# Kernel optimization log

Measured on AMD Instinct MI355X. Metric: run time of the kernel, lower is better.

The kernel has to match this reference:

```python
import jax, jax.numpy as jnp
import numpy as np

PRE_NMS_TOPK = 6000
POST_NMS_TOPK = 1000
NMS_THRESH = 0.7
MIN_SIZE = 16.0
NEG = -1e9  # stand-in for -inf that is safe under autodiff


def setup_inputs() -> dict:
    key = jax.random.key(0)
    k1, k2, k3, k4, k5, k6, k7, k8 = jax.random.split(key, 8)
    B, A = 8, 200000
    N = B * A
    # realistic anchors: centers within a ~1333x800 canvas, sizes 16..256
    cx = jax.random.uniform(k1, (N,), minval=0.0, maxval=1200.0)
    cy = jax.random.uniform(k2, (N,), minval=0.0, maxval=800.0)
    w = jax.random.uniform(k3, (N,), minval=16.0, maxval=256.0)
    h = jax.random.uniform(k4, (N,), minval=16.0, maxval=256.0)
    anchors = jnp.stack([cx - 0.5 * w, cy - 0.5 * h, cx + 0.5 * w, cy + 0.5 * h], axis=1)
    batch_indices = jnp.sort(jax.random.randint(k5, (N,), 0, B)).astype(jnp.int32)
    image_sizes = jax.random.randint(k6, (B, 2), 600, 1334).astype(jnp.int32)  # (H, W)
    objectness_logits = jax.random.normal(k7, (N, 1), dtype=jnp.float32)
    bbox_deltas = jax.random.normal(k8, (N, 4), dtype=jnp.float32) * 0.2
    return {
        'anchors': anchors,
        'batch_indices': batch_indices,
        'image_sizes': image_sizes,
        'objectness_logits': objectness_logits,
        'bbox_deltas': bbox_deltas,
    }


def _nms_one(bx, sc):
    """Greedy NMS on [K,4] boxes / [K] scores; returns POST_NMS_TOPK (idx, ok)."""
    K = bx.shape[0]
    areas = (bx[:, 2] - bx[:, 0]) * (bx[:, 3] - bx[:, 1])
    ar = jnp.arange(K)

    def step(sup, _):
        s = jnp.where(sup, NEG, sc)
        j = jnp.argmax(s)
        ok = s[j] > 0.5 * NEG
        b = bx[j]
        ix1 = jnp.maximum(b[0], bx[:, 0])
        iy1 = jnp.maximum(b[1], bx[:, 1])
        ix2 = jnp.minimum(b[2], bx[:, 2])
        iy2 = jnp.minimum(b[3], bx[:, 3])
        inter = jnp.maximum(ix2 - ix1, 0.0) * jnp.maximum(iy2 - iy1, 0.0)
        iou = inter / (areas + areas[j] - inter + 1e-9)
        sup = sup | (iou > NMS_THRESH) | (ar == j)
        return sup, (j, ok)

    sup0 = sc <= 0.5 * NEG  # padded / invalid entries start suppressed
    _, (idx, ok) = jax.lax.scan(step, sup0, None, length=POST_NMS_TOPK)
    return idx, ok


def reference(anchors, batch_indices, image_sizes, objectness_logits, bbox_deltas):
    B = image_sizes.shape[0]
    N = anchors.shape[0]
    sizes = image_sizes[batch_indices].astype(jnp.float32)  # [N,2] (H,W) per anchor

    # --- box decode ---
    a_w = anchors[:, 2] - anchors[:, 0]
    a_h = anchors[:, 3] - anchors[:, 1]
    a_x = anchors[:, 0] + 0.5 * a_w
    a_y = anchors[:, 1] + 0.5 * a_h
    t_x, t_y = bbox_deltas[:, 0], bbox_deltas[:, 1]
    t_w, t_h = bbox_deltas[:, 2], bbox_deltas[:, 3]
    p_x = a_x + t_x * a_w
    p_y = a_y + t_y * a_h
    p_w = a_w * jnp.exp(jnp.clip(t_w, -10.0, 10.0))
    p_h = a_h * jnp.exp(jnp.clip(t_h, -10.0, 10.0))
    x1 = p_x - 0.5 * p_w
    y1 = p_y - 0.5 * p_h
    x2 = p_x + 0.5 * p_w
    y2 = p_y + 0.5 * p_h

    # --- clip to image ---
    H, W = sizes[:, 0], sizes[:, 1]
    x1 = jnp.clip(x1, 0.0, W - 1.0)
    y1 = jnp.clip(y1, 0.0, H - 1.0)
    x2 = jnp.clip(x2, 0.0, W - 1.0)
    y2 = jnp.clip(y2, 0.0, H - 1.0)
    boxes = jnp.stack([x1, y1, x2, y2], axis=1)  # [N,4]

    # --- min-size filter (as score masking) ---
    valid = ((x2 - x1) >= MIN_SIZE) & ((y2 - y1) >= MIN_SIZE)
    fg = jax.nn.sigmoid(objectness_logits[:, 0])

    # --- per-image top-k over masked scores ---
    img_mask = batch_indices[None, :] == jnp.arange(B, dtype=batch_indices.dtype)[:, None]  # [B,N]
    scores = jnp.where(img_mask & valid[None, :], fg[None, :], NEG)  # [B,N]
    top_scores, top_idx = jax.lax.top_k(scores, PRE_NMS_TOPK)  # [B,PRE]
    top_boxes = boxes[top_idx]  # [B,PRE,4]

    # --- NMS per image ---
    keep_idx, keep_ok = jax.vmap(_nms_one)(top_boxes, top_scores)  # [B,POST]

    sel = jnp.take_along_axis(top_idx, keep_idx, axis=1)  # global anchor indices [B,POST]
    okf = keep_ok[..., None].astype(boxes.dtype)
    props = jnp.take_along_axis(top_boxes, keep_idx[..., None], axis=1) * okf  # [B,POST,4]
    obj = objectness_logits[sel] * okf  # [B,POST,1]
    deltas_out = bbox_deltas[sel] * okf  # [B,POST,4]
    bidx = jnp.where(keep_ok, jnp.arange(B, dtype=jnp.int32)[:, None], -1)  # [B,POST]

    return (props.reshape(-1, 4), bidx.reshape(-1), obj.reshape(-1, 1),
            deltas_out.reshape(-1, 4), keep_ok.reshape(-1))
```

## Files before the change

### kernel.cpp

```cpp
#include <hip/hip_runtime.h>
#include <stdint.h>

#define PRE_K   6000
#define POST_K  1000
#define CAP     8192
#define BINS    1024
#define ROWS    6016
#define CH      94
#define RC_CH   32
#define JSPLIT  4
#define NEGF    -1000000000.0f
#define IOU_EPS 16.0f


__device__ __forceinline__ uint32_t orderf(float f) {
  uint32_t u = __float_as_uint(f);
  return (u & 0x80000000u) ? ~u : (u | 0x80000000u);
}

__device__ __forceinline__ int score_bin(float sc) {
  int bin = (int)floorf((sc + 12.0f) * ((float)BINS / 24.0f));
  return bin < 0 ? 0 : (bin > BINS - 1 ? BINS - 1 : bin);
}

__device__ __forceinline__ int bin_slot(int bin) {
  return ((bin & 15) << 6) | (bin >> 4);
}

__device__ __forceinline__ void decode_box(
    const float* __restrict__ anchors, const float* __restrict__ deltas,
    const int* __restrict__ isz, int n, int b,
    double& x1, double& y1, double& x2, double& y2, bool& valid) {
  double ax1 = (double)anchors[4 * n + 0], ay1 = (double)anchors[4 * n + 1];
  double ax2 = (double)anchors[4 * n + 2], ay2 = (double)anchors[4 * n + 3];
  double aw = ax2 - ax1, ah = ay2 - ay1;
  double acx = ax1 + 0.5 * aw, acy = ay1 + 0.5 * ah;
  double tx = (double)deltas[4 * n + 0], ty = (double)deltas[4 * n + 1];
  double tw = (double)deltas[4 * n + 2], th = (double)deltas[4 * n + 3];
  tw = tw < -10.0 ? -10.0 : (tw > 10.0 ? 10.0 : tw);
  th = th < -10.0 ? -10.0 : (th > 10.0 ? 10.0 : th);
  double px = acx + tx * aw, py = acy + ty * ah;
  double pw = aw * exp(tw), ph = ah * exp(th);
  double H = (double)isz[2 * b + 0], W = (double)isz[2 * b + 1];
  double wm = W - 1.0, hm = H - 1.0;
  x1 = px - 0.5 * pw; y1 = py - 0.5 * ph;
  x2 = px + 0.5 * pw; y2 = py + 0.5 * ph;
  x1 = fmin(fmax(x1, 0.0), wm); x2 = fmin(fmax(x2, 0.0), wm);
  y1 = fmin(fmax(y1, 0.0), hm); y2 = fmin(fmax(y2, 0.0), hm);
  valid = (x2 - x1 >= 16.0) && (y2 - y1 >= 16.0);
}

__device__ __forceinline__ bool iou_exact(const double* __restrict__ tbox,
                                          const double* __restrict__ tarea,
                                          size_t ri, size_t ci) {
  const double* pr = &tbox[ri * 4];
  const double* pc = &tbox[ci * 4];
  double w = fmin(pr[2], pc[2]) - fmax(pr[0], pc[0]); w = w > 0.0 ? w : 0.0;
  double h = fmin(pr[3], pc[3]) - fmax(pr[1], pc[1]); h = h > 0.0 ? h : 0.0;
  double it = w * h;
  return it > 0.7 * (tarea[ri] + tarea[ci] - it + 1e-9);
}


__global__ void k_init(uint32_t* hist, uint32_t* cnt, uint32_t* prank, int B) {
  int i = blockIdx.x * blockDim.x + threadIdx.x;
  if (i < B * BINS) hist[i] = 0u;
  if (i < B) cnt[i] = 0u;
  if (i < B * CAP) prank[i] = 0u;
}

__global__ void __launch_bounds__(256) k_score(const float* __restrict__ anchors,
                                               const int* __restrict__ bix,
                                               const int* __restrict__ isz,
                                               const float* __restrict__ logits,
                                               const float* __restrict__ deltas,
                                               float* __restrict__ scores,
                                               uint32_t* __restrict__ hist, int N) {
  const int SPAN = 4096;
  int start = blockIdx.x * SPAN;
  int end = start + SPAN < N ? start + SPAN : N;
  __shared__ uint32_t lh[2][BINS];
  for (int i = threadIdx.x; i < 2 * BINS; i += 256) ((uint32_t*)lh)[i] = 0u;
  __shared__ int s_b0, s_b1;
  if (threadIdx.x == 0) { s_b0 = bix[start]; s_b1 = bix[end - 1]; }
  __syncthreads();
  int b0 = s_b0, b1 = s_b1;

  for (int n = start + (int)threadIdx.x; n < end; n += 256) {
    int b = bix[n];
    double x1, y1, x2, y2; bool valid;
    decode_box(anchors, deltas, isz, n, b, x1, y1, x2, y2, valid);
    float sc = valid ? logits[n] : NEGF;
    scores[n] = sc;
    if (valid) {
      int bin = score_bin(sc);
      if (b == b0)      atomicAdd(&lh[0][bin], 1u);
      else if (b == b1) atomicAdd(&lh[1][bin], 1u);
      else              atomicAdd(&hist[b * BINS + bin_slot(bin)], 1u);
    }
  }
  __syncthreads();
  for (int bin = threadIdx.x; bin < BINS; bin += 256) {
    uint32_t c0 = lh[0][bin];
    if (c0) atomicAdd(&hist[b0 * BINS + bin_slot(bin)], c0);
    if (b1 != b0) {
      uint32_t c1 = lh[1][bin];
      if (c1) atomicAdd(&hist[b1 * BINS + bin_slot(bin)], c1);
    }
  }
}

__global__ void k_scan(const uint32_t* __restrict__ hist, uint32_t* __restrict__ bstar) {
  __shared__ uint32_t s[BINS];
  __shared__ int bs;
  int b = blockIdx.x, t = threadIdx.x;
  s[t] = hist[b * BINS + bin_slot(t)];
  if (t == 0) bs = 0;
  __syncthreads();
  for (int off = 1; off < BINS; off <<= 1) {
    uint32_t v = (t + off < BINS) ? s[t + off] : 0u;
    __syncthreads();
    s[t] += v;
    __syncthreads();
  }
  if (s[t] >= PRE_K) atomicMax(&bs, t);
  __syncthreads();
  if (t == 0) bstar[b] = (uint32_t)bs;
}

__global__ void __launch_bounds__(1024) k_compact(const float* __restrict__ scores,
                                                  const int* __restrict__ bix,
                                                  const uint32_t* __restrict__ bstar,
                                                  uint32_t* __restrict__ cnt,
                                                  uint64_t* __restrict__ cand, int N) {
  const int SPAN = 8192;
  int start = blockIdx.x * SPAN;
  int end = start + SPAN < N ? start + SPAN : N;
  __shared__ uint32_t lcnt[8], lbase[8];
  if (threadIdx.x < 8) lcnt[threadIdx.x] = 0u;
  __syncthreads();

  bool     predv[8];
  uint64_t keyv[8];
  uint32_t lposv[8];
  int      bv[8];
  int nt = 0;
  for (int base = start; base < end; base += 1024, nt++) {
    int n = base + (int)threadIdx.x;
    bool pred = false; int b = 0; uint64_t key = 0ull; uint32_t lp = 0u;
    if (n < end) {
      float sc = scores[n];
      if (sc > 0.5f * NEGF) {
        b = bix[n];
        if ((uint32_t)score_bin(sc) >= bstar[b]) {
          pred = true;
          key = ((uint64_t)orderf(sc) << 32) | (uint64_t)(uint32_t)(~(uint32_t)n);
          lp = atomicAdd(&lcnt[b], 1u);
        }
      }
    }
    predv[nt] = pred; keyv[nt] = key; lposv[nt] = lp; bv[nt] = b;
  }
  __syncthreads();
  if (threadIdx.x < 8) {
    uint32_t c = lcnt[threadIdx.x];
    lbase[threadIdx.x] = c ? atomicAdd(&cnt[threadIdx.x], c) : 0u;
  }
  __syncthreads();
  for (int k = 0; k < nt; k++) {
    if (predv[k]) {
      uint32_t pos = lbase[bv[k]] + lposv[k];
      if (pos < CAP) cand[(size_t)bv[k] * CAP + pos] = keyv[k];
    }
  }
}

__global__ void __launch_bounds__(256) k_rank(const uint64_t* __restrict__ cand,
                                              const uint32_t* __restrict__ cnt,
                                              uint32_t* __restrict__ prank) {
  int blk = blockIdx.x;
  int js = blk % JSPLIT;
  int ic = (blk / JSPLIT) % 32;
  int b  = blk / (JSPLIT * 32);
  int t = threadIdx.x;
  int C = (int)min(cnt[b], (uint32_t)CAP);
  if (ic * 256 >= C) return;
  const uint64_t* g = cand + (size_t)b * CAP;
  int i = ic * 256 + t;
  uint64_t ki = (i < C) ? g[i] : 0ull;

  int q = (C + JSPLIT - 1) / JSPLIT;
  int j0 = js * q;
  int j1 = j0 + q < C ? j0 + q : C;
  if (j0 >= j1) return;

  __shared__ uint64_t tile[1024];
  int rank = 0;
  for (int base = j0; base < j1; base += 1024) {
#pragma unroll
    for (int u = 0; u < 4; u++) {
      int j = base + u * 256 + t;
      tile[u * 256 + t] = (j < j1) ? g[j] : 0ull;
    }
    __syncthreads();
    int lim = j1 - base < 1024 ? j1 - base : 1024;
    const ulonglong2* t2 = (const ulonglong2*)tile;
    int pairs = lim >> 1;
    int jj = 0;
    for (; jj + 4 <= pairs; jj += 4) {
      ulonglong2 v0 = t2[jj + 0], v1 = t2[jj + 1];
      ulonglong2 v2 = t2[jj + 2], v3 = t2[jj + 3];
      rank += (v0.x > ki) ? 1 : 0; rank += (v0.y > ki) ? 1 : 0;
      rank += (v1.x > ki) ? 1 : 0; rank += (v1.y > ki) ? 1 : 0;
      rank += (v2.x > ki) ? 1 : 0; rank += (v2.y > ki) ? 1 : 0;
      rank += (v3.x > ki) ? 1 : 0; rank += (v3.y > ki) ? 1 : 0;
    }
    for (; jj < pairs; jj++) {
      ulonglong2 v = t2[jj];
      rank += (v.x > ki) ? 1 : 0; rank += (v.y > ki) ? 1 : 0;
    }
    if (lim & 1) rank += (tile[lim - 1] > ki) ? 1 : 0;
    __syncthreads();
  }
  if (i < C && rank) atomicAdd(&prank[b * CAP + i], (uint32_t)rank);
}

__global__ void __launch_bounds__(256) k_place_gather(
    const uint64_t* __restrict__ cand, const uint32_t* __restrict__ cnt,
    const uint32_t* __restrict__ prank,
    const float* __restrict__ anchors, const float* __restrict__ deltas,
    const int* __restrict__ isz,
    double* __restrict__ tbox, double* __restrict__ tarea,
    float4* __restrict__ tboxf, float* __restrict__ tareaf,
    int* __restrict__ top_n, int* __restrict__ Cnum, int B) {
  int idx = blockIdx.x * blockDim.x + threadIdx.x;
  if (idx >= B * CAP) return;
  int b = idx / CAP, i = idx % CAP;
  int C = (int)min(cnt[b], (uint32_t)CAP);
  if (i == 0) Cnum[b] = C < PRE_K ? C : PRE_K;
  if (i >= C) return;
  uint32_t rank = prank[idx];
  if (rank >= PRE_K) return;
  int n = (int)(~(uint32_t)(cand[idx] & 0xFFFFFFFFull));
  double x1, y1, x2, y2; bool valid;
  decode_box(anchors, deltas, isz, n, b, x1, y1, x2, y2, valid);
  size_t row = (size_t)b * ROWS + rank;
  tbox[row * 4 + 0] = x1;
  tbox[row * 4 + 1] = y1;
  tbox[row * 4 + 2] = x2;
  tbox[row * 4 + 3] = y2;
  double ar = (x2 - x1) * (y2 - y1);
  tarea[row] = ar;
  tboxf[row] = make_float4((float)x1, (float)y1, (float)x2, (float)y2);
  tareaf[row] = (float)ar;
  top_n[b * PRE_K + rank] = n;
}

__global__ void __launch_bounds__(64) k_iou_mat(const float4* __restrict__ tboxf,
                                                const float* __restrict__ tareaf,
                                                const double* __restrict__ tbox,
                                                const double* __restrict__ tarea,
                                                const int* __restrict__ Cnum,
                                                uint32_t* __restrict__ maskT) {
  int blk = blockIdx.x;
  int k  = blk % (RC_CH + 1);
  int cc = (blk / (RC_CH + 1)) % CH;
  int b  = blk / ((RC_CH + 1) * CH);
  int rc = (k == RC_CH) ? cc : k;
  if (k < RC_CH && cc <= rc) return;
  int C = Cnum[b];
  if (rc * 64 >= C || cc * 64 >= C) return;
  int lane = threadIdx.x;
  size_t bb = (size_t)b * ROWS;

  float4 cb4 = tboxf[bb + (size_t)cc * 64 + lane];
  float  sca = 0.7f * tareaf[bb + (size_t)cc * 64 + lane];
  __shared__ float4 rbx[64];
  __shared__ float  rsa[64];
  rbx[lane] = tboxf[bb + (size_t)rc * 64 + lane];
  rsa[lane] = 0.7f * tareaf[bb + (size_t)rc * 64 + lane];
  __syncthreads();

  bool isdiag = (rc == cc);
  uint32_t res0 = 0u, res1 = 0u;

  for (int i = 0; i < 64; i++) {
    float4 r4 = rbx[i];
    float sra = rsa[i];
    float iw = fminf(r4.z, cb4.z) - fmaxf(r4.x, cb4.x);
    float ih = fminf(r4.w, cb4.w) - fmaxf(r4.y, cb4.y);
    iw = fmaxf(iw, 0.0f); ih = fmaxf(ih, 0.0f);
    float inter = iw * ih;
    float diff = fmaf(1.7f, inter, -(sra + sca));
    bool gt = isdiag ? (lane > i) : true;
    unsigned long long sup   = __ballot(gt && (diff >  IOU_EPS));
    unsigned long long loose = __ballot(gt && (diff > -IOU_EPS));
    unsigned long long border = loose & ~sup;
    if (border) {
      bool mine = (border >> lane) & 1ull;
      bool ex = false;
      if (mine)
        ex = iou_exact(tbox, tarea, bb + (size_t)rc * 64 + i,
                       bb + (size_t)cc * 64 + lane);
      sup |= __ballot(ex);
    }
    if (lane == i) { res0 = (uint32_t)sup; res1 = (uint32_t)(sup >> 32); }
  }
  uint2* seg = (uint2*)(maskT + (((size_t)b * CH + cc) * ROWS + (size_t)rc * 64) * 2);
  seg[lane] = make_uint2(res0, res1);
}

__global__ void __launch_bounds__(256) k_nms_reduce(const uint32_t* __restrict__ maskT,
                                                    const float4* __restrict__ tboxf,
                                                    const float* __restrict__ tareaf,
                                                    const double* __restrict__ tbox,
                                                    const double* __restrict__ tarea,
                                                    const int* __restrict__ Cnum,
                                                    int* __restrict__ keep,
                                                    int* __restrict__ kept_count) {
  int b = blockIdx.x, t = threadIdx.x;
  int wave = t >> 6, lane = t & 63;
  int C = Cnum[b];
  const uint32_t* M = maskT + (size_t)b * CH * ROWS * 2;
  size_t bb = (size_t)b * ROWS;

  __shared__ uint32_t s_f[2][2];
  __shared__ uint32_t kept_lo[POST_K];
  __shared__ uint32_t kept_hi[POST_K];
  __shared__ uint64_t s_kept;
  if (t < 4) ((uint32_t*)s_f)[t] = 0u;

  uint32_t d0 = 0u, d1 = 0u;
  if (wave == 0) {
    const uint32_t* rp = M + (size_t)lane * 2;
    d0 = rp[0]; d1 = rp[1];
  }
  __syncthreads();

  int nkept = 0, nlo = 0, nhi = 0;
  for (int c = 0; c < CH; c++) {
    int base = c * 64;
    if (base >= C) break;
    int cbuf = c & 1;
    if (t == 0) { s_f[cbuf ^ 1][0] = 0u; s_f[cbuf ^ 1][1] = 0u; }

    uint32_t f0 = 0u, f1 = 0u;
    for (int k2 = t; k2 < nlo; k2 += 256) {
      const uint32_t* rp = M + ((size_t)c * ROWS + kept_lo[k2]) * 2;
      f0 |= rp[0]; f1 |= rp[1];
    }
    if (nhi > 0) {
      float4 cb4 = tboxf[bb + base + lane];
      float  sca = 0.7f * tareaf[bb + base + lane];
      for (int k2 = wave; k2 < nhi; k2 += 4) {
        int r = (int)kept_hi[k2];
        float4 r4 = tboxf[bb + r];
        float sra = 0.7f * tareaf[bb + r];
        float iw = fminf(r4.z, cb4.z) - fmaxf(r4.x, cb4.x);
        float ih = fminf(r4.w, cb4.w) - fmaxf(r4.y, cb4.y);
        iw = fmaxf(iw, 0.0f); ih = fmaxf(ih, 0.0f);
        float inter = iw * ih;
        float diff = fmaf(1.7f, inter, -(sra + sca));
        unsigned long long sup   = __ballot(diff >  IOU_EPS);
        unsigned long long loose = __ballot(diff > -IOU_EPS);
        unsigned long long border = loose & ~sup;
        if (border) {
          bool mine = (border >> lane) & 1ull;
          bool ex = false;
          if (mine) ex = iou_exact(tbox, tarea, bb + r, bb + base + lane);
          sup |= __ballot(ex);
        }
        f0 |= (uint32_t)sup; f1 |= (uint32_t)(sup >> 32);
      }
    }
#pragma unroll
    for (int off = 32; off > 0; off >>= 1) {
      f0 |= (uint32_t)__shfl_xor((int)f0, off, 64);
      f1 |= (uint32_t)__shfl_xor((int)f1, off, 64);
    }
    if (lane == 0 && (f0 | f1)) {
      atomicOr(&s_f[cbuf][0], f0);
      atomicOr(&s_f[cbuf][1], f1);
    }
    __syncthreads();

    if (wave == 0) {
      uint64_t sup = (uint64_t)s_f[cbuf][0] | ((uint64_t)s_f[cbuf][1] << 32);
      int rem = C - base;
      if (rem < 64) sup |= ~((1ull << rem) - 1ull);
      uint64_t diag = (uint64_t)d0 | ((uint64_t)d1 << 32);
      int cn = (c + 1 < CH) ? c + 1 : c;
      const uint32_t* rpn = M + ((size_t)cn * ROWS + (size_t)cn * 64 + lane) * 2;
      uint32_t pn0 = rpn[0], pn1 = rpn[1];

      uint64_t keptMask = 0ull;
      uint64_t alive = ~sup;
      uint64_t m = alive;
      while (m) {
        int i = __builtin_ctzll(m);
        keptMask |= 1ull << i;
        uint64_t d = (uint64_t)__shfl((long long)diag, i, 64);
        sup |= d | (1ull << i);
        m = alive & ~sup;
      }
      int allowed = POST_K - nkept;
      int pc = __popcll(keptMask);
      while (pc > allowed) {
        keptMask &= ~(1ull << (63 - __builtin_clzll(keptMask)));
        pc--;
      }
      if (lane == 0) s_kept = keptMask;
      if ((keptMask >> lane) & 1ull) {
        int pfx = __popcll(keptMask & ((1ull << lane) - 1ull));
        keep[b * POST_K + nkept + pfx] = base + lane;
        if (c < RC_CH) kept_lo[nlo + pfx] = (uint32_t)(base + lane);
        else           kept_hi[nhi + pfx] = (uint32_t)(base + lane);
      }
      d0 = pn0; d1 = pn1;
    }
    __syncthreads();

    int pc = __popcll(s_kept);
    nkept += pc;
    if (c < RC_CH) nlo += pc; else nhi += pc;
    if (nkept >= POST_K) break;
  }
  if (t == 0) kept_count[b] = nkept;
}

__global__ void k_output(const int* __restrict__ keep,
                         const int* __restrict__ kept_count,
                         const int* __restrict__ top_n,
                         const double* __restrict__ tbox,
                         const float* __restrict__ logits,
                         const float* __restrict__ deltas,
                         float* __restrict__ out, int B) {
  int idx = blockIdx.x * blockDim.x + threadIdx.x;
  int M = B * POST_K;
  if (idx >= M) return;
  int b = idx / POST_K, s = idx % POST_K;
  float p0 = 0.f, p1 = 0.f, p2 = 0.f, p3 = 0.f;
  float ob = 0.f, d0 = 0.f, d1 = 0.f, d2 = 0.f, d3 = 0.f;
  float bi = -1.0f, okv = 0.0f;
  if (s < kept_count[b]) {
    int j = keep[b * POST_K + s];
    int n = top_n[b * PRE_K + j];
    const double* p = &tbox[((size_t)b * ROWS + j) * 4];
    p0 = (float)p[0]; p1 = (float)p[1]; p2 = (float)p[2]; p3 = (float)p[3];
    ob = logits[n];
    d0 = deltas[4 * n + 0]; d1 = deltas[4 * n + 1];
    d2 = deltas[4 * n + 2]; d3 = deltas[4 * n + 3];
    bi = (float)b; okv = 1.0f;
  }
  out[idx * 4 + 0] = p0;
  out[idx * 4 + 1] = p1;
  out[idx * 4 + 2] = p2;
  out[idx * 4 + 3] = p3;
  out[4 * M + idx] = bi;
  out[5 * M + idx] = ob;
  out[6 * M + idx * 4 + 0] = d0;
  out[6 * M + idx * 4 + 1] = d1;
  out[6 * M + idx * 4 + 2] = d2;
  out[6 * M + idx * 4 + 3] = d3;
  out[10 * M + idx] = okv;
}


extern "C" void kernel_launch(void* const* d_in, const int* in_sizes, int n_in,
                              void* d_out, int out_size, void* d_ws, size_t ws_size,
                              hipStream_t stream) {
  const float* anchors = (const float*)d_in[0];
  const int*   bix     = (const int*)d_in[1];
  const int*   isz     = (const int*)d_in[2];
  const float* logits  = (const float*)d_in[3];
  const float* deltas  = (const float*)d_in[4];
  float* out = (float*)d_out;

  int N = in_sizes[1];
  int B = in_sizes[2] / 2;

  uintptr_t p = (uintptr_t)d_ws;
  double*   tbox   = (double*)p;    p += (size_t)B * ROWS * 4 * sizeof(double);
  double*   tarea  = (double*)p;    p += (size_t)B * ROWS * sizeof(double);
  uint64_t* cand   = (uint64_t*)p;  p += (size_t)B * CAP * sizeof(uint64_t);
  float*    scores = (float*)p;     p += (size_t)N * sizeof(float);
  uint32_t* hist   = (uint32_t*)p;  p += (size_t)B * BINS * sizeof(uint32_t);
  uint32_t* prank  = (uint32_t*)p;  p += (size_t)B * CAP * sizeof(uint32_t);
  int*      top_n    = (int*)p;     p += (size_t)B * PRE_K * sizeof(int);
  int*      keep     = (int*)p;     p += (size_t)B * POST_K * sizeof(int);
  uint32_t* cnt      = (uint32_t*)p; p += (size_t)B * sizeof(uint32_t);
  uint32_t* bstar    = (uint32_t*)p; p += (size_t)B * sizeof(uint32_t);
  int*      Cnum     = (int*)p;      p += (size_t)B * sizeof(int);
  int*      kept_cnt = (int*)p;      p += (size_t)B * sizeof(int);
  p = (p + 255) & ~(uintptr_t)255;
  uint32_t* maskT    = (uint32_t*)p; p += (size_t)B * CH * ROWS * 2 * sizeof(uint32_t);
  float4*   tboxf  = (float4*)scores;
  float*    tareaf = (float*)(scores + (size_t)B * ROWS * 4);
  (void)ws_size; (void)n_in; (void)out_size;

  int initN = B * CAP;
  k_init<<<(initN + 255) / 256, 256, 0, stream>>>(hist, cnt, prank, B);
  k_score<<<(N + 4095) / 4096, 256, 0, stream>>>(anchors, bix, isz, logits, deltas,
                                                 scores, hist, N);
  k_scan<<<B, BINS, 0, stream>>>(hist, bstar);
  k_compact<<<(N + 8191) / 8192, 1024, 0, stream>>>(scores, bix, bstar, cnt, cand, N);
  k_rank<<<B * 32 * JSPLIT, 256, 0, stream>>>(cand, cnt, prank);
  k_place_gather<<<(B * CAP + 255) / 256, 256, 0, stream>>>(cand, cnt, prank,
                                                            anchors, deltas, isz,
                                                            tbox, tarea, tboxf,
                                                            tareaf, top_n, Cnum, B);
  k_iou_mat<<<B * CH * (RC_CH + 1), 64, 0, stream>>>(tboxf, tareaf, tbox, tarea,
                                                     Cnum, maskT);
  k_nms_reduce<<<B, 256, 0, stream>>>(maskT, tboxf, tareaf, tbox, tarea, Cnum,
                                      keep, kept_cnt);
  k_output<<<(B * POST_K + 255) / 256, 256, 0, stream>>>(keep, kept_cnt, top_n,
                                                         tbox, logits, deltas,
                                                         out, B);
}
```

Baseline: 354.9 us.

## Process four NMS column chunks per block-sync step using precomputed cross masks

The serial NMS reduce now handles four 64-row chunks per iteration instead of one. The IoU-mask kernel additionally computes the off-diagonal masks between nearby high chunks (up to three chunks apart), so the in-chunk greedy pass can propagate suppression across the four chunks. This cuts the number of block-wide barriers and serial iterations by about four. In exchange the IoU-mask kernel launches more blocks, the reduce uses more registers, and the high-chunk IoU loop now runs one wave per chunk instead of splitting kept boxes across waves.

```diff
diff --git a/kernel.cpp b/kernel.cpp
--- a/kernel.cpp
+++ b/kernel.cpp
@@ -7,6 +7,7 @@
 #define BINS    1024
 #define ROWS    6016
 #define CH      94
+#define SCH     ((CH + 3) / 4)
 #define RC_CH   32
 #define JSPLIT  4
 #define NEGF    -1000000000.0f
@@ -25,6 +26,10 @@
 
 __device__ __forceinline__ int bin_slot(int bin) {
   return ((bin & 15) << 6) | (bin >> 4);
+}
+
+__device__ __forceinline__ uint64_t shfl64(uint64_t v, int src) {
+  return (uint64_t)__shfl((long long)v, src, 64);
 }
 
 __device__ __forceinline__ void decode_box(
@@ -263,11 +268,19 @@
                                                 const int* __restrict__ Cnum,
                                                 uint32_t* __restrict__ maskT) {
   int blk = blockIdx.x;
-  int k  = blk % (RC_CH + 1);
-  int cc = (blk / (RC_CH + 1)) % CH;
-  int b  = blk / ((RC_CH + 1) * CH);
-  int rc = (k == RC_CH) ? cc : k;
-  if (k < RC_CH && cc <= rc) return;
+  int k  = blk % (RC_CH + 4);
+  int cc = (blk / (RC_CH + 4)) % CH;
+  int b  = blk / ((RC_CH + 4) * CH);
+  int rc;
+  if (k < RC_CH) {
+    rc = k;
+    if (cc <= rc) return;
+  } else {
+    int j = k - RC_CH;
+    rc = cc - j;
+    if (rc < 0) return;
+    if (j > 0 && rc < RC_CH) return;
+  }
   int C = Cnum[b];
   if (rc * 64 >= C || cc * 64 >= C) return;
   int lane = threadIdx.x;
@@ -324,105 +337,174 @@
   const uint32_t* M = maskT + (size_t)b * CH * ROWS * 2;
   size_t bb = (size_t)b * ROWS;
 
-  __shared__ uint32_t s_f[2][2];
+  __shared__ uint32_t s_f[2][8];
   __shared__ uint32_t kept_lo[POST_K];
   __shared__ uint32_t kept_hi[POST_K];
-  __shared__ uint64_t s_kept;
-  if (t < 4) ((uint32_t*)s_f)[t] = 0u;
-
-  uint32_t d0 = 0u, d1 = 0u;
+  __shared__ int s_cnt[3];
+  if (t < 16) ((uint32_t*)s_f)[t] = 0u;
+
+  uint2 dg[4], cx[6];
   if (wave == 0) {
-    const uint32_t* rp = M + (size_t)lane * 2;
-    d0 = rp[0]; d1 = rp[1];
+#pragma unroll
+    for (int q = 0; q < 4; q++)
+      dg[q] = *(const uint2*)(M + (((size_t)q) * ROWS + (size_t)q * 64 + lane) * 2);
+    int e = 0;
+#pragma unroll
+    for (int q = 0; q < 3; q++)
+#pragma unroll
+      for (int q2 = q + 1; q2 < 4; q2++, e++)
+        cx[e] = *(const uint2*)(M + (((size_t)q2) * ROWS + (size_t)q * 64 + lane) * 2);
   }
   __syncthreads();
 
   int nkept = 0, nlo = 0, nhi = 0;
-  for (int c = 0; c < CH; c++) {
-    int base = c * 64;
-    if (base >= C) break;
-    int cbuf = c & 1;
-    if (t == 0) { s_f[cbuf ^ 1][0] = 0u; s_f[cbuf ^ 1][1] = 0u; }
-
-    uint32_t f0 = 0u, f1 = 0u;
+  for (int s = 0; s < SCH; s++) {
+    int c0 = s * 4;
+    int base0 = c0 * 64;
+    if (base0 >= C) break;
+    int cbuf = s & 1;
+    if (t < 8) s_f[cbuf ^ 1][t] = 0u;
+
+    uint32_t f[8] = {0u, 0u, 0u, 0u, 0u, 0u, 0u, 0u};
     for (int k2 = t; k2 < nlo; k2 += 256) {
-      const uint32_t* rp = M + ((size_t)c * ROWS + kept_lo[k2]) * 2;
-      f0 |= rp[0]; f1 |= rp[1];
-    }
-    if (nhi > 0) {
-      float4 cb4 = tboxf[bb + base + lane];
-      float  sca = 0.7f * tareaf[bb + base + lane];
-      for (int k2 = wave; k2 < nhi; k2 += 4) {
-        int r = (int)kept_hi[k2];
-        float4 r4 = tboxf[bb + r];
-        float sra = 0.7f * tareaf[bb + r];
-        float iw = fminf(r4.z, cb4.z) - fmaxf(r4.x, cb4.x);
-        float ih = fminf(r4.w, cb4.w) - fmaxf(r4.y, cb4.y);
-        iw = fmaxf(iw, 0.0f); ih = fmaxf(ih, 0.0f);
-        float inter = iw * ih;
-        float diff = fmaf(1.7f, inter, -(sra + sca));
-        unsigned long long sup   = __ballot(diff >  IOU_EPS);
-        unsigned long long loose = __ballot(diff > -IOU_EPS);
-        unsigned long long border = loose & ~sup;
-        if (border) {
-          bool mine = (border >> lane) & 1ull;
-          bool ex = false;
-          if (mine) ex = iou_exact(tbox, tarea, bb + r, bb + base + lane);
-          sup |= __ballot(ex);
+      uint32_t r = kept_lo[k2];
+#pragma unroll
+      for (int q = 0; q < 4; q++) {
+        if (base0 + q * 64 < C) {
+          uint2 v = *(const uint2*)(M + (((size_t)(c0 + q)) * ROWS + r) * 2);
+          f[2 * q] |= v.x; f[2 * q + 1] |= v.y;
         }
-        f0 |= (uint32_t)sup; f1 |= (uint32_t)(sup >> 32);
+      }
+    }
+    {
+      int baseq = base0 + wave * 64;
+      if (nhi > 0 && baseq < C) {
+        float4 cb4 = tboxf[bb + baseq + lane];
+        float  sca = 0.7f * tareaf[bb + baseq + lane];
+        for (int k2 = 0; k2 < nhi; k2++) {
+          int r = (int)kept_hi[k2];
+          float4 r4 = tboxf[bb + r];
+          float sra = 0.7f * tareaf[bb + r];
+          float iw = fminf(r4.z, cb4.z) - fmaxf(r4.x, cb4.x);
+          float ih = fminf(r4.w, cb4.w) - fmaxf(r4.y, cb4.y);
+          iw = fmaxf(iw, 0.0f); ih = fmaxf(ih, 0.0f);
+          float inter = iw * ih;
+          float diff = fmaf(1.7f, inter, -(sra + sca));
+          unsigned long long sup   = __ballot(diff >  IOU_EPS);
+          unsigned long long loose = __ballot(diff > -IOU_EPS);
+          unsigned long long border = loose & ~sup;
+          if (border) {
+            bool mine = (border >> lane) & 1ull;
+            bool ex = false;
+            if (mine) ex = iou_exact(tbox, tarea, bb + r, bb + baseq + lane);
+            sup |= __ballot(ex);
+          }
+          f[2 * wave] |= (uint32_t)sup;
+          f[2 * wave + 1] |= (uint32_t)(sup >> 32);
+        }
       }
     }
 #pragma unroll
     for (int off = 32; off > 0; off >>= 1) {
-      f0 |= (uint32_t)__shfl_xor((int)f0, off, 64);
-      f1 |= (uint32_t)__shfl_xor((int)f1, off, 64);
-    }
-    if (lane == 0 && (f0 | f1)) {
-      atomicOr(&s_f[cbuf][0], f0);
-      atomicOr(&s_f[cbuf][1], f1);
+#pragma unroll
+      for (int w = 0; w < 8; w++)
+        f[w] |= (uint32_t)__shfl_xor((int)f[w], off, 64);
+    }
+    if (lane == 0) {
+#pragma unroll
+      for (int w = 0; w < 8; w++)
+        if (f[w]) atomicOr(&s_f[cbuf][w], f[w]);
     }
     __syncthreads();
 
     if (wave == 0) {
-      uint64_t sup = (uint64_t)s_f[cbuf][0] | ((uint64_t)s_f[cbuf][1] << 32);
-      int rem = C - base;
-      if (rem < 64) sup |= ~((1ull << rem) - 1ull);
-      uint64_t diag = (uint64_t)d0 | ((uint64_t)d1 << 32);
-      int cn = (c + 1 < CH) ? c + 1 : c;
-      const uint32_t* rpn = M + ((size_t)cn * ROWS + (size_t)cn * 64 + lane) * 2;
-      uint32_t pn0 = rpn[0], pn1 = rpn[1];
-
-      uint64_t keptMask = 0ull;
-      uint64_t alive = ~sup;
-      uint64_t m = alive;
-      while (m) {
-        int i = __builtin_ctzll(m);
-        keptMask |= 1ull << i;
-        uint64_t d = (uint64_t)__shfl((long long)diag, i, 64);
-        sup |= d | (1ull << i);
-        m = alive & ~sup;
-      }
+      uint64_t sup[4], diag64[4], cross64[6];
+#pragma unroll
+      for (int q = 0; q < 4; q++) {
+        sup[q] = (uint64_t)s_f[cbuf][2 * q] | ((uint64_t)s_f[cbuf][2 * q + 1] << 32);
+        int rem = C - (base0 + q * 64);
+        if (rem <= 0) sup[q] = ~0ull;
+        else if (rem < 64) sup[q] |= ~((1ull << rem) - 1ull);
+        diag64[q] = (uint64_t)dg[q].x | ((uint64_t)dg[q].y << 32);
+      }
+#pragma unroll
+      for (int e = 0; e < 6; e++)
+        cross64[e] = (uint64_t)cx[e].x | ((uint64_t)cx[e].y << 32);
+
+      int c0n = (s + 1 < SCH) ? (s + 1) * 4 : c0;
+      uint2 ndg[4], ncx[6];
+#pragma unroll
+      for (int q = 0; q < 4; q++) {
+        int cc = c0n + q < CH ? c0n + q : CH - 1;
+        ndg[q] = *(const uint2*)(M + (((size_t)cc) * ROWS + (size_t)cc * 64 + lane) * 2);
+      }
+      {
+        int e = 0;
+#pragma unroll
+        for (int q = 0; q < 3; q++)
+#pragma unroll
+          for (int q2 = q + 1; q2 < 4; q2++, e++) {
+            int rc = c0n + q  < CH ? c0n + q  : CH - 1;
+            int cc = c0n + q2 < CH ? c0n + q2 : CH - 1;
+            ncx[e] = *(const uint2*)(M + (((size_t)cc) * ROWS + (size_t)rc * 64 + lane) * 2);
+          }
+      }
+
+      uint64_t keptM[4] = {0ull, 0ull, 0ull, 0ull};
+      static const int xbase[3] = {0, 3, 5};
+#pragma unroll
+      for (int q = 0; q < 4; q++) {
+        uint64_t alive = ~sup[q];
+        uint64_t m = alive;
+        while (m) {
+          int i = __builtin_ctzll(m);
+          keptM[q] |= 1ull << i;
+          sup[q] |= shfl64(diag64[q], i) | (1ull << i);
+          if (q < 3) {
+            int xb = xbase[q];
+            for (int q2 = q + 1; q2 < 4; q2++)
+              sup[q2] |= shfl64(cross64[xb + (q2 - q - 1)], i);
+          }
+          m = alive & ~sup[q];
+        }
+      }
+      int tot = __popcll(keptM[0]) + __popcll(keptM[1]) +
+                __popcll(keptM[2]) + __popcll(keptM[3]);
       int allowed = POST_K - nkept;
-      int pc = __popcll(keptMask);
-      while (pc > allowed) {
-        keptMask &= ~(1ull << (63 - __builtin_clzll(keptMask)));
-        pc--;
-      }
-      if (lane == 0) s_kept = keptMask;
-      if ((keptMask >> lane) & 1ull) {
-        int pfx = __popcll(keptMask & ((1ull << lane) - 1ull));
-        keep[b * POST_K + nkept + pfx] = base + lane;
-        if (c < RC_CH) kept_lo[nlo + pfx] = (uint32_t)(base + lane);
-        else           kept_hi[nhi + pfx] = (uint32_t)(base + lane);
-      }
-      d0 = pn0; d1 = pn1;
+      if (tot > allowed) {
+        for (int q = 3; q >= 0 && tot > allowed; q--) {
+          while (tot > allowed && keptM[q]) {
+            keptM[q] &= ~(1ull << (63 - __builtin_clzll(keptM[q])));
+            tot--;
+          }
+        }
+      }
+      int off = 0, lo_add = 0, hi_add = 0;
+#pragma unroll
+      for (int q = 0; q < 4; q++) {
+        uint64_t km = keptM[q];
+        int pc = __popcll(km);
+        int baseq = base0 + q * 64;
+        bool isLo = baseq < RC_CH * 64;
+        if ((km >> lane) & 1ull) {
+          int pfx = __popcll(km & ((1ull << lane) - 1ull));
+          int row = baseq + lane;
+          keep[b * POST_K + nkept + off + pfx] = row;
+          if (isLo) kept_lo[nlo + lo_add + pfx] = (uint32_t)row;
+          else      kept_hi[nhi + hi_add + pfx] = (uint32_t)row;
+        }
+        off += pc;
+        if (isLo) lo_add += pc; else hi_add += pc;
+      }
+      if (lane == 0) { s_cnt[0] = off; s_cnt[1] = lo_add; s_cnt[2] = hi_add; }
+#pragma unroll
+      for (int q = 0; q < 4; q++) dg[q] = ndg[q];
+#pragma unroll
+      for (int e = 0; e < 6; e++) cx[e] = ncx[e];
     }
     __syncthreads();
 
-    int pc = __popcll(s_kept);
-    nkept += pc;
-    if (c < RC_CH) nlo += pc; else nhi += pc;
+    nkept += s_cnt[0]; nlo += s_cnt[1]; nhi += s_cnt[2];
     if (nkept >= POST_K) break;
   }
   if (t == 0) kept_count[b] = nkept;
@@ -509,7 +591,7 @@
                                                             anchors, deltas, isz,
                                                             tbox, tarea, tboxf,
                                                             tareaf, top_n, Cnum, B);
-  k_iou_mat<<<B * CH * (RC_CH + 1), 64, 0, stream>>>(tboxf, tareaf, tbox, tarea,
+  k_iou_mat<<<B * CH * (RC_CH + 4), 64, 0, stream>>>(tboxf, tareaf, tbox, tarea,
                                                      Cnum, maskT);
   k_nms_reduce<<<B, 256, 0, stream>>>(maskT, tboxf, tareaf, tbox, tarea, Cnum,
                                       keep, kept_cnt);
```

Result: slower. 402.3 us (+13.3%).

## Process two NMS chunks per serial step and fuse output gathering into reduce kernel

Applied to the files above, without the earlier changes.

The serial NMS reduce loop now handles two 64-box chunks per iteration. It precomputes the cross-chunk mask block for the high chunks in the IoU kernel, which halves the number of block-wide barriers and scalar-loop round trips. Kept indices stay in shared memory, and the output gather is fused into the reduce kernel, which removes one launch and the keep buffer round trip. In exchange, the IoU kernel launches more blocks and the single wave does more sequential shuffle work per step.

```diff
diff --git a/kernel.cpp b/kernel.cpp
--- a/kernel.cpp
+++ b/kernel.cpp
@@ -7,6 +7,7 @@
 #define BINS    1024
 #define ROWS    6016
 #define CH      94
+#define SCH2    (CH / 2)
 #define RC_CH   32
 #define JSPLIT  4
 #define NEGF    -1000000000.0f
@@ -25,6 +26,10 @@
 
 __device__ __forceinline__ int bin_slot(int bin) {
   return ((bin & 15) << 6) | (bin >> 4);
+}
+
+__device__ __forceinline__ uint64_t shfl64(uint64_t v, int src) {
+  return (uint64_t)__shfl((long long)v, src, 64);
 }
 
 __device__ __forceinline__ void decode_box(
@@ -263,11 +268,19 @@
                                                 const int* __restrict__ Cnum,
                                                 uint32_t* __restrict__ maskT) {
   int blk = blockIdx.x;
-  int k  = blk % (RC_CH + 1);
-  int cc = (blk / (RC_CH + 1)) % CH;
-  int b  = blk / ((RC_CH + 1) * CH);
-  int rc = (k == RC_CH) ? cc : k;
-  if (k < RC_CH && cc <= rc) return;
+  int k  = blk % (RC_CH + 2);
+  int cc = (blk / (RC_CH + 2)) % CH;
+  int b  = blk / ((RC_CH + 2) * CH);
+  int rc;
+  if (k < RC_CH) {
+    rc = k;
+    if (cc <= rc) return;
+  } else if (k == RC_CH) {
+    rc = cc;
+  } else {
+    rc = cc - 1;
+    if (rc < RC_CH) return;
+  }
   int C = Cnum[b];
   if (rc * 64 >= C || cc * 64 >= C) return;
   int lane = threadIdx.x;
@@ -316,153 +329,196 @@
                                                     const double* __restrict__ tbox,
                                                     const double* __restrict__ tarea,
                                                     const int* __restrict__ Cnum,
-                                                    int* __restrict__ keep,
-                                                    int* __restrict__ kept_count) {
+                                                    const int* __restrict__ top_n,
+                                                    const float* __restrict__ logits,
+                                                    const float* __restrict__ deltas,
+                                                    float* __restrict__ out, int B) {
   int b = blockIdx.x, t = threadIdx.x;
   int wave = t >> 6, lane = t & 63;
   int C = Cnum[b];
   const uint32_t* M = maskT + (size_t)b * CH * ROWS * 2;
   size_t bb = (size_t)b * ROWS;
 
-  __shared__ uint32_t s_f[2][2];
+  __shared__ uint32_t s_f[2][4];
   __shared__ uint32_t kept_lo[POST_K];
   __shared__ uint32_t kept_hi[POST_K];
-  __shared__ uint64_t s_kept;
-  if (t < 4) ((uint32_t*)s_f)[t] = 0u;
-
-  uint32_t d0 = 0u, d1 = 0u;
+  __shared__ int s_cnt[3];
+  if (t < 8) ((uint32_t*)s_f)[t] = 0u;
+
+  uint2 dg0, dg1, cx;
   if (wave == 0) {
-    const uint32_t* rp = M + (size_t)lane * 2;
-    d0 = rp[0]; d1 = rp[1];
+    dg0 = *(const uint2*)(M + ((size_t)0 * ROWS + (size_t)0 * 64 + lane) * 2);
+    dg1 = *(const uint2*)(M + ((size_t)1 * ROWS + (size_t)1 * 64 + lane) * 2);
+    cx  = *(const uint2*)(M + ((size_t)1 * ROWS + (size_t)0 * 64 + lane) * 2);
   }
   __syncthreads();
 
   int nkept = 0, nlo = 0, nhi = 0;
-  for (int c = 0; c < CH; c++) {
-    int base = c * 64;
-    if (base >= C) break;
-    int cbuf = c & 1;
-    if (t == 0) { s_f[cbuf ^ 1][0] = 0u; s_f[cbuf ^ 1][1] = 0u; }
-
-    uint32_t f0 = 0u, f1 = 0u;
+  for (int s = 0; s < SCH2; s++) {
+    int c0 = s * 2;
+    int base0 = c0 * 64;
+    if (base0 >= C) break;
+    bool has2 = (base0 + 64) < C;
+    int cbuf = s & 1;
+    if (t < 4) s_f[cbuf ^ 1][t] = 0u;
+
+    uint32_t f0 = 0u, f1 = 0u, f2 = 0u, f3 = 0u;
     for (int k2 = t; k2 < nlo; k2 += 256) {
-      const uint32_t* rp = M + ((size_t)c * ROWS + kept_lo[k2]) * 2;
-      f0 |= rp[0]; f1 |= rp[1];
+      uint32_t r = kept_lo[k2];
+      uint2 v0 = *(const uint2*)(M + (((size_t)c0) * ROWS + r) * 2);
+      f0 |= v0.x; f1 |= v0.y;
+      if (has2) {
+        uint2 v1 = *(const uint2*)(M + (((size_t)(c0 + 1)) * ROWS + r) * 2);
+        f2 |= v1.x; f3 |= v1.y;
+      }
     }
     if (nhi > 0) {
-      float4 cb4 = tboxf[bb + base + lane];
-      float  sca = 0.7f * tareaf[bb + base + lane];
-      for (int k2 = wave; k2 < nhi; k2 += 4) {
-        int r = (int)kept_hi[k2];
-        float4 r4 = tboxf[bb + r];
-        float sra = 0.7f * tareaf[bb + r];
-        float iw = fminf(r4.z, cb4.z) - fmaxf(r4.x, cb4.x);
-        float ih = fminf(r4.w, cb4.w) - fmaxf(r4.y, cb4.y);
-        iw = fmaxf(iw, 0.0f); ih = fmaxf(ih, 0.0f);
-        float inter = iw * ih;
-        float diff = fmaf(1.7f, inter, -(sra + sca));
-        unsigned long long sup   = __ballot(diff >  IOU_EPS);
-        unsigned long long loose = __ballot(diff > -IOU_EPS);
-        unsigned long long border = loose & ~sup;
-        if (border) {
-          bool mine = (border >> lane) & 1ull;
-          bool ex = false;
-          if (mine) ex = iou_exact(tbox, tarea, bb + r, bb + base + lane);
-          sup |= __ballot(ex);
+      int q = wave & 1, half = wave >> 1;
+      int baseq = base0 + q * 64;
+      if (baseq < C) {
+        float4 cb4 = tboxf[bb + baseq + lane];
+        float  sca = 0.7f * tareaf[bb + baseq + lane];
+        for (int k2 = half; k2 < nhi; k2 += 2) {
+          int r = (int)kept_hi[k2];
+          float4 r4 = tboxf[bb + r];
+          float sra = 0.7f * tareaf[bb + r];
+          float iw = fminf(r4.z, cb4.z) - fmaxf(r4.x, cb4.x);
+          float ih = fminf(r4.w, cb4.w) - fmaxf(r4.y, cb4.y);
+          iw = fmaxf(iw, 0.0f); ih = fmaxf(ih, 0.0f);
+          float inter = iw * ih;
+          float diff = fmaf(1.7f, inter, -(sra + sca));
+          unsigned long long sup   = __ballot(diff >  IOU_EPS);
+          unsigned long long loose = __ballot(diff > -IOU_EPS);
+          unsigned long long border = loose & ~sup;
+          if (border) {
+            bool mine = (border >> lane) & 1ull;
+            bool ex = false;
+            if (mine) ex = iou_exact(tbox, tarea, bb + r, bb + baseq + lane);
+            sup |= __ballot(ex);
+          }
+          if (q == 0) { f0 |= (uint32_t)sup; f1 |= (uint32_t)(sup >> 32); }
+          else        { f2 |= (uint32_t)sup; f3 |= (uint32_t)(sup >> 32); }
         }
-        f0 |= (uint32_t)sup; f1 |= (uint32_t)(sup >> 32);
       }
     }
 #pragma unroll
     for (int off = 32; off > 0; off >>= 1) {
       f0 |= (uint32_t)__shfl_xor((int)f0, off, 64);
       f1 |= (uint32_t)__shfl_xor((int)f1, off, 64);
-    }
-    if (lane == 0 && (f0 | f1)) {
-      atomicOr(&s_f[cbuf][0], f0);
-      atomicOr(&s_f[cbuf][1], f1);
+      f2 |= (uint32_t)__shfl_xor((int)f2, off, 64);
+      f3 |= (uint32_t)__shfl_xor((int)f3, off, 64);
+    }
+    if (lane == 0) {
+      if (f0) atomicOr(&s_f[cbuf][0], f0);
+      if (f1) atomicOr(&s_f[cbuf][1], f1);
+      if (f2) atomicOr(&s_f[cbuf][2], f2);
+      if (f3) atomicOr(&s_f[cbuf][3], f3);
     }
     __syncthreads();
 
     if (wave == 0) {
-      uint64_t sup = (uint64_t)s_f[cbuf][0] | ((uint64_t)s_f[cbuf][1] << 32);
-      int rem = C - base;
-      if (rem < 64) sup |= ~((1ull << rem) - 1ull);
-      uint64_t diag = (uint64_t)d0 | ((uint64_t)d1 << 32);
-      int cn = (c + 1 < CH) ? c + 1 : c;
-      const uint32_t* rpn = M + ((size_t)cn * ROWS + (size_t)cn * 64 + lane) * 2;
-      uint32_t pn0 = rpn[0], pn1 = rpn[1];
-
-      uint64_t keptMask = 0ull;
-      uint64_t alive = ~sup;
-      uint64_t m = alive;
-      while (m) {
-        int i = __builtin_ctzll(m);
-        keptMask |= 1ull << i;
-        uint64_t d = (uint64_t)__shfl((long long)diag, i, 64);
-        sup |= d | (1ull << i);
-        m = alive & ~sup;
-      }
+      uint64_t sup0 = (uint64_t)s_f[cbuf][0] | ((uint64_t)s_f[cbuf][1] << 32);
+      uint64_t sup1 = (uint64_t)s_f[cbuf][2] | ((uint64_t)s_f[cbuf][3] << 32);
+      {
+        int rem0 = C - base0;
+        if (rem0 < 64) sup0 |= ~((1ull << rem0) - 1ull);
+        int rem1 = C - (base0 + 64);
+        if (rem1 <= 0) sup1 = ~0ull;
+        else if (rem1 < 64) sup1 |= ~((1ull << rem1) - 1ull);
+      }
+      uint64_t diag0 = (uint64_t)dg0.x | ((uint64_t)dg0.y << 32);
+      uint64_t diag1 = (uint64_t)dg1.x | ((uint64_t)dg1.y << 32);
+      uint64_t cross = (uint64_t)cx.x | ((uint64_t)cx.y << 32);
+      int c0n = (s + 1 < SCH2) ? (s + 1) * 2 : c0;
+      uint2 ndg0 = *(const uint2*)(M + (((size_t)c0n) * ROWS + (size_t)c0n * 64 + lane) * 2);
+      uint2 ndg1 = *(const uint2*)(M + (((size_t)(c0n + 1)) * ROWS + (size_t)(c0n + 1) * 64 + lane) * 2);
+      uint2 ncx  = *(const uint2*)(M + (((size_t)(c0n + 1)) * ROWS + (size_t)c0n * 64 + lane) * 2);
+
+      uint64_t kept0 = 0ull, kept1 = 0ull;
+      {
+        uint64_t alive = ~sup0, m = alive;
+        while (m) {
+          int i = __builtin_ctzll(m);
+          kept0 |= 1ull << i;
+          sup0 |= shfl64(diag0, i) | (1ull << i);
+          sup1 |= shfl64(cross, i);
+          m = alive & ~sup0;
+        }
+      }
+      {
+        uint64_t alive = ~sup1, m = alive;
+        while (m) {
+          int i = __builtin_ctzll(m);
+          kept1 |= 1ull << i;
+          sup1 |= shfl64(diag1, i) | (1ull << i);
+          m = alive & ~sup1;
+        }
+      }
+      int tot = __popcll(kept0) + __popcll(kept1);
       int allowed = POST_K - nkept;
-      int pc = __popcll(keptMask);
-      while (pc > allowed) {
-        keptMask &= ~(1ull << (63 - __builtin_clzll(keptMask)));
-        pc--;
-      }
-      if (lane == 0) s_kept = keptMask;
-      if ((keptMask >> lane) & 1ull) {
-        int pfx = __popcll(keptMask & ((1ull << lane) - 1ull));
-        keep[b * POST_K + nkept + pfx] = base + lane;
-        if (c < RC_CH) kept_lo[nlo + pfx] = (uint32_t)(base + lane);
-        else           kept_hi[nhi + pfx] = (uint32_t)(base + lane);
-      }
-      d0 = pn0; d1 = pn1;
+      while (tot > allowed && kept1) {
+        kept1 &= ~(1ull << (63 - __builtin_clzll(kept1))); tot--;
+      }
+      while (tot > allowed && kept0) {
+        kept0 &= ~(1ull << (63 - __builtin_clzll(kept0))); tot--;
+      }
+      bool isLo = base0 < RC_CH * 64;
+      int pc0 = __popcll(kept0);
+      if ((kept0 >> lane) & 1ull) {
+        int pfx = __popcll(kept0 & ((1ull << lane) - 1ull));
+        int row = base0 + lane;
+        if (isLo) kept_lo[nlo + pfx] = (uint32_t)row;
+        else      kept_hi[nhi + pfx] = (uint32_t)row;
+      }
+      if ((kept1 >> lane) & 1ull) {
+        int pfx = pc0 + __popcll(kept1 & ((1ull << lane) - 1ull));
+        int row = base0 + 64 + lane;
+        if (isLo) kept_lo[nlo + pfx] = (uint32_t)row;
+        else      kept_hi[nhi + pfx] = (uint32_t)row;
+      }
+      if (lane == 0) {
+        int pc = pc0 + __popcll(kept1);
+        s_cnt[0] = pc;
+        s_cnt[1] = isLo ? pc : 0;
+        s_cnt[2] = isLo ? 0 : pc;
+      }
+      dg0 = ndg0; dg1 = ndg1; cx = ncx;
     }
     __syncthreads();
 
-    int pc = __popcll(s_kept);
-    nkept += pc;
-    if (c < RC_CH) nlo += pc; else nhi += pc;
+    nkept += s_cnt[0]; nlo += s_cnt[1]; nhi += s_cnt[2];
     if (nkept >= POST_K) break;
   }
-  if (t == 0) kept_count[b] = nkept;
-}
-
-__global__ void k_output(const int* __restrict__ keep,
-                         const int* __restrict__ kept_count,
-                         const int* __restrict__ top_n,
-                         const double* __restrict__ tbox,
-                         const float* __restrict__ logits,
-                         const float* __restrict__ deltas,
-                         float* __restrict__ out, int B) {
-  int idx = blockIdx.x * blockDim.x + threadIdx.x;
-  int M = B * POST_K;
-  if (idx >= M) return;
-  int b = idx / POST_K, s = idx % POST_K;
-  float p0 = 0.f, p1 = 0.f, p2 = 0.f, p3 = 0.f;
-  float ob = 0.f, d0 = 0.f, d1 = 0.f, d2 = 0.f, d3 = 0.f;
-  float bi = -1.0f, okv = 0.0f;
-  if (s < kept_count[b]) {
-    int j = keep[b * POST_K + s];
-    int n = top_n[b * PRE_K + j];
-    const double* p = &tbox[((size_t)b * ROWS + j) * 4];
-    p0 = (float)p[0]; p1 = (float)p[1]; p2 = (float)p[2]; p3 = (float)p[3];
-    ob = logits[n];
-    d0 = deltas[4 * n + 0]; d1 = deltas[4 * n + 1];
-    d2 = deltas[4 * n + 2]; d3 = deltas[4 * n + 3];
-    bi = (float)b; okv = 1.0f;
-  }
-  out[idx * 4 + 0] = p0;
-  out[idx * 4 + 1] = p1;
-  out[idx * 4 + 2] = p2;
-  out[idx * 4 + 3] = p3;
-  out[4 * M + idx] = bi;
-  out[5 * M + idx] = ob;
-  out[6 * M + idx * 4 + 0] = d0;
-  out[6 * M + idx * 4 + 1] = d1;
-  out[6 * M + idx * 4 + 2] = d2;
-  out[6 * M + idx * 4 + 3] = d3;
-  out[10 * M + idx] = okv;
+
+  __syncthreads();
+  int M_out = B * POST_K;
+  for (int s2 = t; s2 < POST_K; s2 += 256) {
+    float p0 = 0.f, p1 = 0.f, p2 = 0.f, p3 = 0.f;
+    float ob = 0.f, d0 = 0.f, d1 = 0.f, d2 = 0.f, d3 = 0.f;
+    float bi = -1.0f, okv = 0.0f;
+    if (s2 < nkept) {
+      int j = (s2 < nlo) ? (int)kept_lo[s2] : (int)kept_hi[s2 - nlo];
+      int n = top_n[b * PRE_K + j];
+      const double* p = &tbox[(bb + j) * 4];
+      p0 = (float)p[0]; p1 = (float)p[1]; p2 = (float)p[2]; p3 = (float)p[3];
+      ob = logits[n];
+      d0 = deltas[4 * n + 0]; d1 = deltas[4 * n + 1];
+      d2 = deltas[4 * n + 2]; d3 = deltas[4 * n + 3];
+      bi = (float)b; okv = 1.0f;
+    }
+    int idx = b * POST_K + s2;
+    out[idx * 4 + 0] = p0;
+    out[idx * 4 + 1] = p1;
+    out[idx * 4 + 2] = p2;
+    out[idx * 4 + 3] = p3;
+    out[4 * M_out + idx] = bi;
+    out[5 * M_out + idx] = ob;
+    out[6 * M_out + idx * 4 + 0] = d0;
+    out[6 * M_out + idx * 4 + 1] = d1;
+    out[6 * M_out + idx * 4 + 2] = d2;
+    out[6 * M_out + idx * 4 + 3] = d3;
+    out[10 * M_out + idx] = okv;
+  }
 }
 
 
@@ -487,11 +543,9 @@
   uint32_t* hist   = (uint32_t*)p;  p += (size_t)B * BINS * sizeof(uint32_t);
   uint32_t* prank  = (uint32_t*)p;  p += (size_t)B * CAP * sizeof(uint32_t);
   int*      top_n    = (int*)p;     p += (size_t)B * PRE_K * sizeof(int);
-  int*      keep     = (int*)p;     p += (size_t)B * POST_K * sizeof(int);
   uint32_t* cnt      = (uint32_t*)p; p += (size_t)B * sizeof(uint32_t);
   uint32_t* bstar    = (uint32_t*)p; p += (size_t)B * sizeof(uint32_t);
   int*      Cnum     = (int*)p;      p += (size_t)B * sizeof(int);
-  int*      kept_cnt = (int*)p;      p += (size_t)B * sizeof(int);
   p = (p + 255) & ~(uintptr_t)255;
   uint32_t* maskT    = (uint32_t*)p; p += (size_t)B * CH * ROWS * 2 * sizeof(uint32_t);
   float4*   tboxf  = (float4*)scores;
@@ -509,11 +563,8 @@
                                                             anchors, deltas, isz,
                                                             tbox, tarea, tboxf,
                                                             tareaf, top_n, Cnum, B);
-  k_iou_mat<<<B * CH * (RC_CH + 1), 64, 0, stream>>>(tboxf, tareaf, tbox, tarea,
+  k_iou_mat<<<B * CH * (RC_CH + 2), 64, 0, stream>>>(tboxf, tareaf, tbox, tarea,
                                                      Cnum, maskT);
   k_nms_reduce<<<B, 256, 0, stream>>>(maskT, tboxf, tareaf, tbox, tarea, Cnum,
-                                      keep, kept_cnt);
-  k_output<<<(B * POST_K + 255) / 256, 256, 0, stream>>>(keep, kept_cnt, top_n,
-                                                         tbox, logits, deltas,
-                                                         out, B);
-}
+                                      top_n, logits, deltas, out, B);
+}
```

After: 362.4 us. 2.1% more time.
